# Optimization experiments

Hardware: AMD Instinct MI355X
Metric: run time of the kernel (lower is better)

Reference implementation:

```python
import jax, jax.numpy as jnp
import numpy as np

DIM = 128
N_ITER = 8
L_SIZE = 80000
C_SIZE = 120000
N_EDGES = 480000


def _mlp(x, w1, b1, w2, b2):
    # 2-layer MLP with ReLU (satbench_n_mlp_layers=2, activation='relu')
    return jnp.maximum(x @ w1 + b1, 0.0) @ w2 + b2


def _layer_norm(x, g, b, eps=1e-5):
    mu = jnp.mean(x, axis=-1, keepdims=True)
    var = jnp.var(x, axis=-1, keepdims=True)
    return (x - mu) * jax.lax.rsqrt(var + eps) * g + b


def _ln_lstm_cell(x, h, c, wi, wh, g_ih, b_ih, g_hh, b_hh, g_c, b_c):
    # LayerNormBasicLSTMCell: LN on input/hidden gate pre-activations and on new cell state
    gates = _layer_norm(x @ wi, g_ih, b_ih) + _layer_norm(h @ wh, g_hh, b_hh)
    i, f, g, o = jnp.split(gates, 4, axis=1)
    new_c = jax.nn.sigmoid(f) * c + jax.nn.sigmoid(i) * jnp.tanh(g)
    new_h = jax.nn.sigmoid(o) * jnp.tanh(_layer_norm(new_c, g_c, b_c))
    return new_h, new_c


def setup_inputs() -> dict:
    key = jax.random.key(0)
    ks = jax.random.split(key, 24)
    d = DIM
    s1 = 1.0 / np.sqrt(d)
    s2 = 1.0 / np.sqrt(2 * d)
    inp = {
        'l_size': L_SIZE,
        'c_size': C_SIZE,
        'l_edge_index': jax.random.randint(ks[0], (N_EDGES,), 0, L_SIZE),
        'c_edge_index': jax.random.randint(ks[1], (N_EDGES,), 0, C_SIZE),
        'l_emb': jax.random.normal(ks[2], (L_SIZE, d), jnp.float32),
        'c_emb': jax.random.normal(ks[3], (C_SIZE, d), jnp.float32),
        # l2c message MLP
        'l2c_w1': jax.random.normal(ks[4], (d, d), jnp.float32) * s1,
        'l2c_b1': jnp.zeros((d,), jnp.float32),
        'l2c_w2': jax.random.normal(ks[5], (d, d), jnp.float32) * s1,
        'l2c_b2': jnp.zeros((d,), jnp.float32),
        # c2l message MLP
        'c2l_w1': jax.random.normal(ks[6], (d, d), jnp.float32) * s1,
        'c2l_b1': jnp.zeros((d,), jnp.float32),
        'c2l_w2': jax.random.normal(ks[7], (d, d), jnp.float32) * s1,
        'c2l_b2': jnp.zeros((d,), jnp.float32),
        # clause update LSTM (input=d)
        'cu_wi': jax.random.normal(ks[8], (d, 4 * d), jnp.float32) * s1,
        'cu_wh': jax.random.normal(ks[9], (d, 4 * d), jnp.float32) * s1,
        'cu_g_ih': jnp.ones((4 * d,), jnp.float32),
        'cu_b_ih': jnp.zeros((4 * d,), jnp.float32),
        'cu_g_hh': jnp.ones((4 * d,), jnp.float32),
        'cu_b_hh': jnp.zeros((4 * d,), jnp.float32),
        'cu_g_c': jnp.ones((d,), jnp.float32),
        'cu_b_c': jnp.zeros((d,), jnp.float32),
        # literal update LSTM (input=2*d)
        'lu_wi': jax.random.normal(ks[10], (2 * d, 4 * d), jnp.float32) * s2,
        'lu_wh': jax.random.normal(ks[11], (d, 4 * d), jnp.float32) * s1,
        'lu_g_ih': jnp.ones((4 * d,), jnp.float32),
        'lu_b_ih': jnp.zeros((4 * d,), jnp.float32),
        'lu_g_hh': jnp.ones((4 * d,), jnp.float32),
        'lu_b_hh': jnp.zeros((4 * d,), jnp.float32),
        'lu_g_c': jnp.ones((d,), jnp.float32),
        'lu_b_c': jnp.zeros((d,), jnp.float32),
    }
    return inp


def reference(l_size, c_size, l_edge_index, c_edge_index, l_emb, c_emb,
              l2c_w1, l2c_b1, l2c_w2, l2c_b2,
              c2l_w1, c2l_b1, c2l_w2, c2l_b2,
              cu_wi, cu_wh, cu_g_ih, cu_b_ih, cu_g_hh, cu_b_hh, cu_g_c, cu_b_c,
              lu_wi, lu_wh, lu_g_ih, lu_b_ih, lu_g_hh, lu_b_hh, lu_g_c, lu_b_c):
    d = l_emb.shape[1]
    l_state = jnp.zeros((l_size, d), l_emb.dtype)
    c_state = jnp.zeros((c_size, d), c_emb.dtype)
    l_embs = [l_emb]
    c_embs = [c_emb]
    for _ in range(N_ITER):
        # literal -> clause
        l_msg_feat = _mlp(l_emb, l2c_w1, l2c_b1, l2c_w2, l2c_b2)
        l2c_msg = l_msg_feat[l_edge_index]                             # [E, d] gather
        l2c_aggr = jax.ops.segment_sum(l2c_msg, c_edge_index, num_segments=c_size)
        c_emb, c_state = _ln_lstm_cell(l2c_aggr, c_emb, c_state,
                                       cu_wi, cu_wh, cu_g_ih, cu_b_ih,
                                       cu_g_hh, cu_b_hh, cu_g_c, cu_b_c)
        c_embs.append(c_emb)
        # clause -> literal
        c_msg_feat = _mlp(c_emb, c2l_w1, c2l_b1, c2l_w2, c2l_b2)
        c2l_msg = c_msg_feat[c_edge_index]
        c2l_aggr = jax.ops.segment_sum(c2l_msg, l_edge_index, num_segments=l_size)
        # flip pos/neg literal embeddings (l2l message)
        pl, ul = jnp.split(l_emb.reshape(l_size // 2, 2 * d), 2, axis=1)
        l2l_msg = jnp.concatenate([ul, pl], axis=1).reshape(l_size, d)
        l_emb, l_state = _ln_lstm_cell(jnp.concatenate([c2l_aggr, l2l_msg], axis=1),
                                       l_emb, l_state,
                                       lu_wi, lu_wh, lu_g_ih, lu_b_ih,
                                       lu_g_hh, lu_b_hh, lu_g_c, lu_b_c)
        l_embs.append(l_emb)
    return jnp.stack(l_embs), jnp.stack(c_embs)
```

## Files before the change

### kernel.cpp

```cpp
#include <hip/hip_runtime.h>
#include <hip/hip_bf16.h>

#define L_SIZE 80000
#define C_SIZE 120000
#define N_EDGES 480000
#define DIM 128
#define GDIM 512
#define N_ITER 8
#define MAXDEG 64

typedef __attribute__((ext_vector_type(8))) short short8;
typedef __attribute__((ext_vector_type(4))) float f32x4;

__device__ __forceinline__ ushort f2bf(float f) {
    uint u = __float_as_uint(f);
    u = u + 0x7FFFu + ((u >> 16) & 1u);
    return (ushort)(u >> 16);
}
__device__ __forceinline__ float bf2f(ushort h) {
    return __uint_as_float(((uint)h) << 16);
}
__device__ __forceinline__ void split2(float f, short& hi, short& lo) {
    uint u = __float_as_uint(f);
    hi = (short)(u >> 16);
    float r = f - __uint_as_float(u & 0xFFFF0000u);
    lo = (short)(__float_as_uint(r) >> 16);
}
__device__ __forceinline__ float sigmf(float x) { return 1.f / (1.f + __expf(-x)); }
__device__ __forceinline__ float tanh_f(float x) {
    float e = __expf(2.f * x);
    return 1.f - 2.f / (e + 1.f);
}
__device__ __forceinline__ f32x4 fzero4() {
    f32x4 v; v[0] = v[1] = v[2] = v[3] = 0.f; return v;
}

__global__ __launch_bounds__(256) void fill_ell(
    const int* __restrict__ src, const int* __restrict__ dst,
    int* __restrict__ cnt, int* __restrict__ ell)
{
    int i = blockIdx.x * 256 + threadIdx.x;
    int d = dst[i];
    int pos = atomicAdd(&cnt[d], 1);
    ell[(size_t)d * MAXDEG + pos] = src[i];
}

__global__ __launch_bounds__(256) void pack_w2(const float* __restrict__ W,
                                               ushort* __restrict__ Ph,
                                               ushort* __restrict__ Pl, int K, int N)
{
    int NC = N / 16;
    int total = K * N;
    for (int o = blockIdx.x * 256 + threadIdx.x; o < total; o += gridDim.x * 256) {
        int j = o & 7, hi = (o >> 3) & 3, c = (o >> 5) & 15;
        int rest = o >> 9;
        int cc = rest % NC, ks = rest / NC;
        int row = ks * 32 + hi * 8 + j, col = cc * 16 + c;
        float v = W[(size_t)row * N + col];
        ushort h = f2bf(v);
        Ph[o] = h;
        Pl[o] = f2bf(v - bf2f(h));
    }
}

__device__ __forceinline__ void stageA2(const float* __restrict__ src, int rowBase,
                                        ushort* dst, int tid, int nrows)
{
    const int planeB = nrows * 256;
    for (int idx = tid * 8; idx < nrows * 128; idx += 512 * 8) {
        int r = idx >> 7, k8 = idx & 127;
        const float* p = src + (size_t)(rowBase + r) * DIM + k8;
        float4 v0 = *(const float4*)p;
        float4 v1 = *(const float4*)(p + 4);
        float f[8] = {v0.x, v0.y, v0.z, v0.w, v1.x, v1.y, v1.z, v1.w};
        short8 hi8, lo8;
        #pragma unroll
        for (int j = 0; j < 8; ++j) {
            short h, l;
            split2(f[j], h, l);
            hi8[j] = h;
            lo8[j] = l;
        }
        int boff = r * 256 + ((k8 * 2) ^ ((r & 7) << 4));
        *(short8*)((char*)dst + boff) = hi8;
        *(short8*)((char*)dst + planeB + boff) = lo8;
    }
}

__device__ __forceinline__ short8 readA(const ushort* As, int mi, int k0, int lane)
{
    int r = mi * 16 + (lane & 15);
    int kb = (k0 * 2 + ((lane >> 4) << 4)) ^ ((r & 7) << 4);
    return *(const short8*)((const char*)As + r * 256 + kb);
}

__device__ __forceinline__ short8 readAf(const ushort* As, int mi, int k0, int lane)
{
    int r = (mi * 16 + (lane & 15)) ^ 1;
    int kb = (k0 * 2 + ((lane >> 4) << 4)) ^ ((r & 7) << 4);
    return *(const short8*)((const char*)As + r * 256 + kb);
}

__device__ __forceinline__ short8 readB(const ushort* P, int ks, int NC, int cc,
                                        int laneOff)
{
    return *(const short8*)((const char*)P + (((size_t)(ks * NC + cc)) << 10) + laneOff);
}

#define MFMA3(acc, ah, al, bh, bl)                                              \
    acc = __builtin_amdgcn_mfma_f32_16x16x32_bf16(ah, bh, acc, 0, 0, 0);        \
    acc = __builtin_amdgcn_mfma_f32_16x16x32_bf16(ah, bl, acc, 0, 0, 0);        \
    acc = __builtin_amdgcn_mfma_f32_16x16x32_bf16(al, bh, acc, 0, 0, 0);

__global__ __launch_bounds__(512, 4) void mlp_kernel(
    const float* __restrict__ A,
    const ushort* __restrict__ w1Ph, const ushort* __restrict__ w1Pl,
    const float* __restrict__ b1,
    const ushort* __restrict__ w2Ph, const ushort* __restrict__ w2Pl,
    const float* __restrict__ b2,
    float* __restrict__ msg)
{
    __shared__ __align__(16) ushort AsIn[2 * 64 * 128];
    __shared__ __align__(16) ushort AsHid[2 * 64 * 128];
    const int tid = threadIdx.x;
    const int wv = tid >> 6, lane = tid & 63;
    const int cl = lane & 15, hi = lane >> 4;
    const int rowBase = blockIdx.x * 64;
    const int laneOff = (cl * 4 + hi) * 16;
    const int col = wv * 16 + cl;

    stageA2(A, rowBase, AsIn, tid, 64);
    float b1c = b1[col], b2c = b2[col];
    __syncthreads();

    f32x4 acc[4];
    #pragma unroll
    for (int mi = 0; mi < 4; ++mi) acc[mi] = fzero4();
    #pragma unroll
    for (int ks = 0; ks < 4; ++ks) {
        short8 bh = readB(w1Ph, ks, 8, wv, laneOff);
        short8 bl = readB(w1Pl, ks, 8, wv, laneOff);
        #pragma unroll
        for (int mi = 0; mi < 4; ++mi) {
            short8 ah = readA(AsIn, mi, ks * 32, lane);
            short8 al = readA(AsIn + 64 * 128, mi, ks * 32, lane);
            MFMA3(acc[mi], ah, al, bh, bl);
        }
    }
    #pragma unroll
    for (int mi = 0; mi < 4; ++mi)
        #pragma unroll
        for (int q = 0; q < 4; ++q) {
            int row = mi * 16 + hi * 4 + q;
            float v = fmaxf(acc[mi][q] + b1c, 0.f);
            short h2, l2;
            split2(v, h2, l2);
            int boff = row * 256 + ((2 * col) ^ ((row & 7) << 4));
            *(short*)((char*)AsHid + boff) = h2;
            *(short*)((char*)AsHid + 64 * 256 + boff) = l2;
        }
    __syncthreads();

    f32x4 acc2[4];
    #pragma unroll
    for (int mi = 0; mi < 4; ++mi) acc2[mi] = fzero4();
    #pragma unroll
    for (int ks = 0; ks < 4; ++ks) {
        short8 bh = readB(w2Ph, ks, 8, wv, laneOff);
        short8 bl = readB(w2Pl, ks, 8, wv, laneOff);
        #pragma unroll
        for (int mi = 0; mi < 4; ++mi) {
            short8 ah = readA(AsHid, mi, ks * 32, lane);
            short8 al = readA(AsHid + 64 * 128, mi, ks * 32, lane);
            MFMA3(acc2[mi], ah, al, bh, bl);
        }
    }
    #pragma unroll
    for (int mi = 0; mi < 4; ++mi)
        #pragma unroll
        for (int q = 0; q < 4; ++q) {
            int row = mi * 16 + hi * 4 + q;
            msg[(size_t)(rowBase + row) * DIM + col] = acc2[mi][q] + b2c;
        }
}

template<int KX>
__global__ __launch_bounds__(512, 4) void lstm_kernel(
    const float* __restrict__ msg, const int* __restrict__ cnt,
    const int* __restrict__ ell,
    const float* __restrict__ Hsrc,
    const ushort* __restrict__ wiPh, const ushort* __restrict__ wiPl,
    const ushort* __restrict__ whPh, const ushort* __restrict__ whPl,
    const float* __restrict__ g_ih, const float* __restrict__ b_ih,
    const float* __restrict__ g_hh, const float* __restrict__ b_hh,
    const float* __restrict__ g_c,  const float* __restrict__ b_c,
    float* __restrict__ c_state, float* __restrict__ h_out)
{
    __shared__ __align__(16) ushort AsX0[2 * 32 * 128];
    __shared__ __align__(16) ushort AsH [2 * 32 * 128];
    __shared__ float Cs[32][132];
    __shared__ float red4f[32 * 33];
    __shared__ float lnstf[32 * 4];
    __shared__ float red2f[32 * 17];
    __shared__ float lncf[32 * 2];

    const int tid = threadIdx.x;
    const int wv = tid >> 6, lane = tid & 63;
    const int cl = lane & 15, hi = lane >> 4;
    const int rowBase = blockIdx.x * 32;
    const int laneOff = (cl * 4 + hi) * 16;
    const int d = wv * 16 + cl;

    stageA2(Hsrc, rowBase, AsH, tid, 32);
    {
        #pragma unroll
        for (int idx = tid * 4; idx < 32 * 128; idx += 512 * 4) {
            int r = idx >> 7, c = idx & 127;
            *(float4*)&Cs[r][c] =
                *(const float4*)(c_state + (size_t)(rowBase + r) * DIM + c);
        }
    }

    {
        int r = tid >> 4;
        int d8 = (tid & 15) << 3;
        int row = rowBase + r;
        int deg = cnt[row];
        const int* sl = ell + (size_t)row * MAXDEG;
        float a0=0,a1=0,a2=0,a3=0,a4=0,a5=0,a6=0,a7=0;
        for (int k = 0; k < deg; k += 4) {
            int i0 = sl[k], i1 = sl[k+1], i2 = sl[k+2], i3 = sl[k+3];
            const float* m0 = msg + (size_t)i0 * DIM + d8;
            const float* m1 = msg + (size_t)i1 * DIM + d8;
            const float* m2 = msg + (size_t)i2 * DIM + d8;
            const float* m3 = msg + (size_t)i3 * DIM + d8;
            float4 p00 = *(const float4*)m0,       p01 = *(const float4*)(m0 + 4);
            float4 p10 = *(const float4*)m1,       p11 = *(const float4*)(m1 + 4);
            float4 p20 = *(const float4*)m2,       p21 = *(const float4*)(m2 + 4);
            float4 p30 = *(const float4*)m3,       p31 = *(const float4*)(m3 + 4);
            float w1 = (k + 1 < deg) ? 1.f : 0.f;
            float w2 = (k + 2 < deg) ? 1.f : 0.f;
            float w3 = (k + 3 < deg) ? 1.f : 0.f;
            a0 += p00.x; a1 += p00.y; a2 += p00.z; a3 += p00.w;
            a4 += p01.x; a5 += p01.y; a6 += p01.z; a7 += p01.w;
            a0 += w1 * p10.x; a1 += w1 * p10.y; a2 += w1 * p10.z; a3 += w1 * p10.w;
            a4 += w1 * p11.x; a5 += w1 * p11.y; a6 += w1 * p11.z; a7 += w1 * p11.w;
            a0 += w2 * p20.x; a1 += w2 * p20.y; a2 += w2 * p20.z; a3 += w2 * p20.w;
            a4 += w2 * p21.x; a5 += w2 * p21.y; a6 += w2 * p21.z; a7 += w2 * p21.w;
            a0 += w3 * p30.x; a1 += w3 * p30.y; a2 += w3 * p30.z; a3 += w3 * p30.w;
            a4 += w3 * p31.x; a5 += w3 * p31.y; a6 += w3 * p31.z; a7 += w3 * p31.w;
        }
        float f[8] = {a0,a1,a2,a3,a4,a5,a6,a7};
        short8 hi8, lo8;
        #pragma unroll
        for (int j = 0; j < 8; ++j) {
            short h, l;
            split2(f[j], h, l);
            hi8[j] = h;
            lo8[j] = l;
        }
        int boff = r * 256 + ((d8 * 2) ^ ((r & 7) << 4));
        *(short8*)((char*)AsX0 + boff) = hi8;
        *(short8*)((char*)AsX0 + 32 * 256 + boff) = lo8;
    }

    float gih[4], bih[4], ghh[4], bhh[4];
    #pragma unroll
    for (int jb = 0; jb < 4; ++jb) {
        int col = jb * 128 + d;
        gih[jb] = g_ih[col]; bih[jb] = b_ih[col];
        ghh[jb] = g_hh[col]; bhh[jb] = b_hh[col];
    }
    const float gcv = g_c[d], bcv = b_c[d];
    __syncthreads();

    f32x4 xacc[2][4], hacc[2][4];
    #pragma unroll
    for (int mi = 0; mi < 2; ++mi)
        #pragma unroll
        for (int jb = 0; jb < 4; ++jb) { xacc[mi][jb] = fzero4(); hacc[mi][jb] = fzero4(); }

    #pragma unroll
    for (int ks = 0; ks < KX; ++ks) {
        int k0 = (ks & 3) * 32;
        short8 axh0, axl0, axh1, axl1;
        if (KX == 8 && ks >= 4) {
            axh0 = readAf(AsH, 0, k0, lane);
            axl0 = readAf(AsH + 32 * 128, 0, k0, lane);
            axh1 = readAf(AsH, 1, k0, lane);
            axl1 = readAf(AsH + 32 * 128, 1, k0, lane);
        } else {
            axh0 = readA(AsX0, 0, k0, lane);
            axl0 = readA(AsX0 + 32 * 128, 0, k0, lane);
            axh1 = readA(AsX0, 1, k0, lane);
            axl1 = readA(AsX0 + 32 * 128, 1, k0, lane);
        }
        #pragma unroll
        for (int jb = 0; jb < 4; ++jb) {
            short8 bh = readB(wiPh, ks, 32, jb * 8 + wv, laneOff);
            short8 bl = readB(wiPl, ks, 32, jb * 8 + wv, laneOff);
            MFMA3(xacc[0][jb], axh0, axl0, bh, bl);
            MFMA3(xacc[1][jb], axh1, axl1, bh, bl);
        }
        if (ks < 4) {
            short8 ahh0 = readA(AsH, 0, k0, lane);
            short8 ahl0 = readA(AsH + 32 * 128, 0, k0, lane);
            short8 ahh1 = readA(AsH, 1, k0, lane);
            short8 ahl1 = readA(AsH + 32 * 128, 1, k0, lane);
            #pragma unroll
            for (int jb = 0; jb < 4; ++jb) {
                short8 bh = readB(whPh, ks, 32, jb * 8 + wv, laneOff);
                short8 bl = readB(whPl, ks, 32, jb * 8 + wv, laneOff);
                MFMA3(hacc[0][jb], ahh0, ahl0, bh, bl);
                MFMA3(hacc[1][jb], ahh1, ahl1, bh, bl);
            }
        }
    }

    #pragma unroll
    for (int mi = 0; mi < 2; ++mi)
        #pragma unroll
        for (int q = 0; q < 4; ++q) {
            float px = 0.f, pqx = 0.f, ph = 0.f, pqh = 0.f;
            #pragma unroll
            for (int jb = 0; jb < 4; ++jb) {
                float v = xacc[mi][jb][q]; px += v; pqx += v * v;
                float u = hacc[mi][jb][q]; ph += u; pqh += u * u;
            }
            #pragma unroll
            for (int m = 1; m < 16; m <<= 1) {
                px += __shfl_xor(px, m); pqx += __shfl_xor(pqx, m);
                ph += __shfl_xor(ph, m); pqh += __shfl_xor(pqh, m);
            }
            if (cl == 0) {
                int row = mi * 16 + hi * 4 + q;
                float* rp = red4f + row * 33 + wv * 4;
                rp[0] = px; rp[1] = pqx; rp[2] = ph; rp[3] = pqh;
            }
        }
    __syncthreads();
    if (tid < 32) {
        float sx = 0.f, qx = 0.f, sh = 0.f, qh = 0.f;
        const float* rp = red4f + tid * 33;
        for (int ww = 0; ww < 8; ++ww) {
            sx += rp[ww * 4 + 0]; qx += rp[ww * 4 + 1];
            sh += rp[ww * 4 + 2]; qh += rp[ww * 4 + 3];
        }
        const float inv = 1.f / 512.f;
        float mux = sx * inv, muh = sh * inv;
        lnstf[tid * 4 + 0] = mux;
        lnstf[tid * 4 + 1] = rsqrtf(qx * inv - mux * mux + 1e-5f);
        lnstf[tid * 4 + 2] = muh;
        lnstf[tid * 4 + 3] = rsqrtf(qh * inv - muh * muh + 1e-5f);
    }
    __syncthreads();

    float cn[2][4], og[2][4];
    #pragma unroll
    for (int mi = 0; mi < 2; ++mi)
        #pragma unroll
        for (int q = 0; q < 4; ++q) {
            int row = mi * 16 + hi * 4 + q;
            float mux = lnstf[row * 4 + 0], rx = lnstf[row * 4 + 1];
            float muh = lnstf[row * 4 + 2], rh = lnstf[row * 4 + 3];
            float g4[4];
            #pragma unroll
            for (int jb = 0; jb < 4; ++jb)
                g4[jb] = (xacc[mi][jb][q] - mux) * rx * gih[jb] + bih[jb]
                       + (hacc[mi][jb][q] - muh) * rh * ghh[jb] + bhh[jb];
            float cp = Cs[row][d];
            float cv = sigmf(g4[1]) * cp + sigmf(g4[0]) * tanh_f(g4[2]);
            cn[mi][q] = cv; og[mi][q] = g4[3];
            float sc = cv, qc = cv * cv;
            #pragma unroll
            for (int m = 1; m < 16; m <<= 1) {
                sc += __shfl_xor(sc, m); qc += __shfl_xor(qc, m);
            }
            if (cl == 0) {
                float* rp = red2f + row * 17 + wv * 2;
                rp[0] = sc; rp[1] = qc;
            }
        }
    __syncthreads();
    if (tid < 32) {
        float sc = 0.f, qc = 0.f;
        const float* rp = red2f + tid * 17;
        for (int ww = 0; ww < 8; ++ww) { sc += rp[ww * 2]; qc += rp[ww * 2 + 1]; }
        const float inv = 1.f / 128.f;
        float mu = sc * inv;
        lncf[tid * 2 + 0] = mu;
        lncf[tid * 2 + 1] = rsqrtf(qc * inv - mu * mu + 1e-5f);
    }
    __syncthreads();

    #pragma unroll
    for (int mi = 0; mi < 2; ++mi)
        #pragma unroll
        for (int q = 0; q < 4; ++q) {
            int row = mi * 16 + hi * 4 + q;
            size_t go = (size_t)(rowBase + row) * DIM + d;
            float cv = cn[mi][q];
            float hv = sigmf(og[mi][q]) *
                       tanh_f((cv - lncf[row * 2]) * lncf[row * 2 + 1] * gcv + bcv);
            c_state[go] = cv;
            h_out[go] = hv;
        }
}

extern "C" void kernel_launch(void* const* d_in, const int* in_sizes, int n_in,
                              void* d_out, int out_size, void* d_ws, size_t ws_size,
                              hipStream_t stream)
{
    const int*   l_edge  = (const int*)d_in[2];
    const int*   c_edge  = (const int*)d_in[3];
    const float* l_emb0  = (const float*)d_in[4];
    const float* c_emb0  = (const float*)d_in[5];
    const float* l2c_w1  = (const float*)d_in[6];
    const float* l2c_b1  = (const float*)d_in[7];
    const float* l2c_w2  = (const float*)d_in[8];
    const float* l2c_b2  = (const float*)d_in[9];
    const float* c2l_w1  = (const float*)d_in[10];
    const float* c2l_b1  = (const float*)d_in[11];
    const float* c2l_w2  = (const float*)d_in[12];
    const float* c2l_b2  = (const float*)d_in[13];
    const float* cu_wi   = (const float*)d_in[14];
    const float* cu_wh   = (const float*)d_in[15];
    const float* cu_g_ih = (const float*)d_in[16];
    const float* cu_b_ih = (const float*)d_in[17];
    const float* cu_g_hh = (const float*)d_in[18];
    const float* cu_b_hh = (const float*)d_in[19];
    const float* cu_g_c  = (const float*)d_in[20];
    const float* cu_b_c  = (const float*)d_in[21];
    const float* lu_wi   = (const float*)d_in[22];
    const float* lu_wh   = (const float*)d_in[23];
    const float* lu_g_ih = (const float*)d_in[24];
    const float* lu_b_ih = (const float*)d_in[25];
    const float* lu_g_hh = (const float*)d_in[26];
    const float* lu_b_hh = (const float*)d_in[27];
    const float* lu_g_c  = (const float*)d_in[28];
    const float* lu_b_c  = (const float*)d_in[29];

    float* out = (float*)d_out;
    float* l_slab = out;
    float* c_slab = out + (size_t)9 * L_SIZE * DIM;

    char* wp = (char*)d_ws;
    float*  l_state = (float*)wp;  wp += (size_t)L_SIZE * DIM * 4;
    float*  c_state = (float*)wp;  wp += (size_t)C_SIZE * DIM * 4;
    float*  msg     = (float*)wp;  wp += (size_t)C_SIZE * DIM * 4;
    int* c_cnt = (int*)wp; wp += C_SIZE * 4;
    int* l_cnt = (int*)wp; wp += L_SIZE * 4;
    int* c_ell = (int*)wp; wp += (size_t)C_SIZE * MAXDEG * 4;
    int* l_ell = (int*)wp; wp += (size_t)L_SIZE * MAXDEG * 4;
    ushort* l2c_w1Ph = (ushort*)wp; wp += 128 * 128 * 2;
    ushort* l2c_w1Pl = (ushort*)wp; wp += 128 * 128 * 2;
    ushort* l2c_w2Ph = (ushort*)wp; wp += 128 * 128 * 2;
    ushort* l2c_w2Pl = (ushort*)wp; wp += 128 * 128 * 2;
    ushort* c2l_w1Ph = (ushort*)wp; wp += 128 * 128 * 2;
    ushort* c2l_w1Pl = (ushort*)wp; wp += 128 * 128 * 2;
    ushort* c2l_w2Ph = (ushort*)wp; wp += 128 * 128 * 2;
    ushort* c2l_w2Pl = (ushort*)wp; wp += 128 * 128 * 2;
    ushort* cu_wiPh  = (ushort*)wp; wp += 128 * 512 * 2;
    ushort* cu_wiPl  = (ushort*)wp; wp += 128 * 512 * 2;
    ushort* cu_whPh  = (ushort*)wp; wp += 128 * 512 * 2;
    ushort* cu_whPl  = (ushort*)wp; wp += 128 * 512 * 2;
    ushort* lu_wiPh  = (ushort*)wp; wp += 256 * 512 * 2;
    ushort* lu_wiPl  = (ushort*)wp; wp += 256 * 512 * 2;
    ushort* lu_whPh  = (ushort*)wp; wp += 128 * 512 * 2;
    ushort* lu_whPl  = (ushort*)wp; wp += 128 * 512 * 2;

    const int eb = N_EDGES / 256;

    hipMemsetAsync(c_cnt, 0, C_SIZE * 4, stream);
    hipMemsetAsync(l_cnt, 0, L_SIZE * 4, stream);
    hipMemsetAsync(c_ell, 0, (size_t)C_SIZE * MAXDEG * 4, stream);
    hipMemsetAsync(l_ell, 0, (size_t)L_SIZE * MAXDEG * 4, stream);
    fill_ell<<<eb, 256, 0, stream>>>(l_edge, c_edge, c_cnt, c_ell);
    fill_ell<<<eb, 256, 0, stream>>>(c_edge, l_edge, l_cnt, l_ell);

    pack_w2<<<64, 256, 0, stream>>>(l2c_w1, l2c_w1Ph, l2c_w1Pl, 128, 128);
    pack_w2<<<64, 256, 0, stream>>>(l2c_w2, l2c_w2Ph, l2c_w2Pl, 128, 128);
    pack_w2<<<64, 256, 0, stream>>>(c2l_w1, c2l_w1Ph, c2l_w1Pl, 128, 128);
    pack_w2<<<64, 256, 0, stream>>>(c2l_w2, c2l_w2Ph, c2l_w2Pl, 128, 128);
    pack_w2<<<256, 256, 0, stream>>>(cu_wi, cu_wiPh, cu_wiPl, 128, 512);
    pack_w2<<<256, 256, 0, stream>>>(cu_wh, cu_whPh, cu_whPl, 128, 512);
    pack_w2<<<512, 256, 0, stream>>>(lu_wi, lu_wiPh, lu_wiPl, 256, 512);
    pack_w2<<<256, 256, 0, stream>>>(lu_wh, lu_whPh, lu_whPl, 128, 512);

    hipMemcpyAsync(l_slab, l_emb0, (size_t)L_SIZE * DIM * sizeof(float),
                   hipMemcpyDeviceToDevice, stream);
    hipMemcpyAsync(c_slab, c_emb0, (size_t)C_SIZE * DIM * sizeof(float),
                   hipMemcpyDeviceToDevice, stream);
    hipMemsetAsync(l_state, 0, (size_t)L_SIZE * DIM * sizeof(float), stream);
    hipMemsetAsync(c_state, 0, (size_t)C_SIZE * DIM * sizeof(float), stream);

    for (int t = 0; t < N_ITER; ++t) {
        const float* le = l_slab + (size_t)t * L_SIZE * DIM;
        const float* ce = c_slab + (size_t)t * C_SIZE * DIM;
        float* le1 = l_slab + (size_t)(t + 1) * L_SIZE * DIM;
        float* ce1 = c_slab + (size_t)(t + 1) * C_SIZE * DIM;

        mlp_kernel<<<L_SIZE / 64, 512, 0, stream>>>(le, l2c_w1Ph, l2c_w1Pl, l2c_b1,
                                                    l2c_w2Ph, l2c_w2Pl, l2c_b2, msg);
        lstm_kernel<4><<<C_SIZE / 32, 512, 0, stream>>>(
            msg, c_cnt, c_ell, ce,
            cu_wiPh, cu_wiPl, cu_whPh, cu_whPl,
            cu_g_ih, cu_b_ih, cu_g_hh, cu_b_hh, cu_g_c, cu_b_c,
            c_state, ce1);

        mlp_kernel<<<C_SIZE / 64, 512, 0, stream>>>(ce1, c2l_w1Ph, c2l_w1Pl, c2l_b1,
                                                    c2l_w2Ph, c2l_w2Pl, c2l_b2, msg);
        lstm_kernel<8><<<L_SIZE / 32, 512, 0, stream>>>(
            msg, l_cnt, l_ell, le,
            lu_wiPh, lu_wiPl, lu_whPh, lu_whPl,
            lu_g_ih, lu_b_ih, lu_g_hh, lu_b_hh, lu_g_c, lu_b_c,
            l_state, le1);
    }
}
```

Baseline: 5.372 ms.

## Double LSTM row tile to 64 rows to halve weight reloads per row

```diff
diff --git a/kernel.cpp b/kernel.cpp
--- a/kernel.cpp
+++ b/kernel.cpp
@@ -108,9 +108,11 @@
 }
 
 #define MFMA3(acc, ah, al, bh, bl)                                              \
-    acc = __builtin_amdgcn_mfma_f32_16x16x32_bf16(ah, bh, acc, 0, 0, 0);        \
-    acc = __builtin_amdgcn_mfma_f32_16x16x32_bf16(ah, bl, acc, 0, 0, 0);        \
-    acc = __builtin_amdgcn_mfma_f32_16x16x32_bf16(al, bh, acc, 0, 0, 0);
+    do {                                                                        \
+        acc = __builtin_amdgcn_mfma_f32_16x16x32_bf16(ah, bh, acc, 0, 0, 0);    \
+        acc = __builtin_amdgcn_mfma_f32_16x16x32_bf16(ah, bl, acc, 0, 0, 0);    \
+        acc = __builtin_amdgcn_mfma_f32_16x16x32_bf16(al, bh, acc, 0, 0, 0);    \
+    } while (0)
 
 __global__ __launch_bounds__(512, 4) void mlp_kernel(
     const float* __restrict__ A,
@@ -185,7 +187,7 @@
 }
 
 template<int KX>
-__global__ __launch_bounds__(512, 4) void lstm_kernel(
+__global__ __launch_bounds__(512, 2) void lstm_kernel(
     const float* __restrict__ msg, const int* __restrict__ cnt,
     const int* __restrict__ ell,
     const float* __restrict__ Hsrc,
@@ -196,72 +198,69 @@
     const float* __restrict__ g_c,  const float* __restrict__ b_c,
     float* __restrict__ c_state, float* __restrict__ h_out)
 {
-    __shared__ __align__(16) ushort AsX0[2 * 32 * 128];
-    __shared__ __align__(16) ushort AsH [2 * 32 * 128];
-    __shared__ float Cs[32][132];
-    __shared__ float red4f[32 * 33];
-    __shared__ float lnstf[32 * 4];
-    __shared__ float red2f[32 * 17];
-    __shared__ float lncf[32 * 2];
+    __shared__ __align__(16) ushort AsX0[2 * 64 * 128];
+    __shared__ __align__(16) ushort AsH [2 * 64 * 128];
+    __shared__ float red4f[64 * 33];
+    __shared__ float lnstf[64 * 4];
+    __shared__ float red2f[64 * 17];
+    __shared__ float lncf[64 * 2];
 
     const int tid = threadIdx.x;
     const int wv = tid >> 6, lane = tid & 63;
     const int cl = lane & 15, hi = lane >> 4;
-    const int rowBase = blockIdx.x * 32;
+    const int rowBase = blockIdx.x * 64;
     const int laneOff = (cl * 4 + hi) * 16;
     const int d = wv * 16 + cl;
 
-    stageA2(Hsrc, rowBase, AsH, tid, 32);
+    stageA2(Hsrc, rowBase, AsH, tid, 64);
+
     {
-        #pragma unroll
-        for (int idx = tid * 4; idx < 32 * 128; idx += 512 * 4) {
-            int r = idx >> 7, c = idx & 127;
-            *(float4*)&Cs[r][c] =
-                *(const float4*)(c_state + (size_t)(rowBase + r) * DIM + c);
-        }
-    }
-
-    {
-        int r = tid >> 4;
-        int d8 = (tid & 15) << 3;
+        int r = tid >> 3;
+        int d16 = (tid & 7) << 4;
         int row = rowBase + r;
         int deg = cnt[row];
         const int* sl = ell + (size_t)row * MAXDEG;
-        float a0=0,a1=0,a2=0,a3=0,a4=0,a5=0,a6=0,a7=0;
-        for (int k = 0; k < deg; k += 4) {
-            int i0 = sl[k], i1 = sl[k+1], i2 = sl[k+2], i3 = sl[k+3];
-            const float* m0 = msg + (size_t)i0 * DIM + d8;
-            const float* m1 = msg + (size_t)i1 * DIM + d8;
-            const float* m2 = msg + (size_t)i2 * DIM + d8;
-            const float* m3 = msg + (size_t)i3 * DIM + d8;
-            float4 p00 = *(const float4*)m0,       p01 = *(const float4*)(m0 + 4);
-            float4 p10 = *(const float4*)m1,       p11 = *(const float4*)(m1 + 4);
-            float4 p20 = *(const float4*)m2,       p21 = *(const float4*)(m2 + 4);
-            float4 p30 = *(const float4*)m3,       p31 = *(const float4*)(m3 + 4);
+        float a[16];
+        #pragma unroll
+        for (int j = 0; j < 16; ++j) a[j] = 0.f;
+        for (int k = 0; k < deg; k += 2) {
+            int i0 = sl[k], i1 = sl[k + 1];
+            const float* m0 = msg + (size_t)i0 * DIM + d16;
+            const float* m1 = msg + (size_t)i1 * DIM + d16;
+            float4 p00 = *(const float4*)m0,        p01 = *(const float4*)(m0 + 4);
+            float4 p02 = *(const float4*)(m0 + 8),  p03 = *(const float4*)(m0 + 12);
+            float4 p10 = *(const float4*)m1,        p11 = *(const float4*)(m1 + 4);
+            float4 p12 = *(const float4*)(m1 + 8),  p13 = *(const float4*)(m1 + 12);
             float w1 = (k + 1 < deg) ? 1.f : 0.f;
-            float w2 = (k + 2 < deg) ? 1.f : 0.f;
-            float w3 = (k + 3 < deg) ? 1.f : 0.f;
-            a0 += p00.x; a1 += p00.y; a2 += p00.z; a3 += p00.w;
-            a4 += p01.x; a5 += p01.y; a6 += p01.z; a7 += p01.w;
-            a0 += w1 * p10.x; a1 += w1 * p10.y; a2 += w1 * p10.z; a3 += w1 * p10.w;
-            a4 += w1 * p11.x; a5 += w1 * p11.y; a6 += w1 * p11.z; a7 += w1 * p11.w;
-            a0 += w2 * p20.x; a1 += w2 * p20.y; a2 += w2 * p20.z; a3 += w2 * p20.w;
-            a4 += w2 * p21.x; a5 += w2 * p21.y; a6 += w2 * p21.z; a7 += w2 * p21.w;
-            a0 += w3 * p30.x; a1 += w3 * p30.y; a2 += w3 * p30.z; a3 += w3 * p30.w;
-            a4 += w3 * p31.x; a5 += w3 * p31.y; a6 += w3 * p31.z; a7 += w3 * p31.w;
-        }
-        float f[8] = {a0,a1,a2,a3,a4,a5,a6,a7};
-        short8 hi8, lo8;
+            a[0]  += p00.x; a[1]  += p00.y; a[2]  += p00.z; a[3]  += p00.w;
+            a[4]  += p01.x; a[5]  += p01.y; a[6]  += p01.z; a[7]  += p01.w;
+            a[8]  += p02.x; a[9]  += p02.y; a[10] += p02.z; a[11] += p02.w;
+            a[12] += p03.x; a[13] += p03.y; a[14] += p03.z; a[15] += p03.w;
+            a[0]  += w1 * p10.x; a[1]  += w1 * p10.y; a[2]  += w1 * p10.z; a[3]  += w1 * p10.w;
+            a[4]  += w1 * p11.x; a[5]  += w1 * p11.y; a[6]  += w1 * p11.z; a[7]  += w1 * p11.w;
+            a[8]  += w1 * p12.x; a[9]  += w1 * p12.y; a[10] += w1 * p12.z; a[11] += w1 * p12.w;
+            a[12] += w1 * p13.x; a[13] += w1 * p13.y; a[14] += w1 * p13.z; a[15] += w1 * p13.w;
+        }
+        int sw = (r & 7) << 4;
+        short8 hiA, loA, hiB, loB;
         #pragma unroll
         for (int j = 0; j < 8; ++j) {
             short h, l;
-            split2(f[j], h, l);
-            hi8[j] = h;
-            lo8[j] = l;
-        }
-        int boff = r * 256 + ((d8 * 2) ^ ((r & 7) << 4));
-        *(short8*)((char*)AsX0 + boff) = hi8;
-        *(short8*)((char*)AsX0 + 32 * 256 + boff) = lo8;
+            split2(a[j], h, l);
+            hiA[j] = h; loA[j] = l;
+        }
+        #pragma unroll
+        for (int j = 0; j < 8; ++j) {
+            short h, l;
+            split2(a[8 + j], h, l);
+            hiB[j] = h; loB[j] = l;
+        }
+        int b0 = r * 256 + ((d16 * 2) ^ sw);
+        int b1 = r * 256 + (((d16 + 8) * 2) ^ sw);
+        *(short8*)((char*)AsX0 + b0) = hiA;
+        *(short8*)((char*)AsX0 + b1) = hiB;
+        *(short8*)((char*)AsX0 + 64 * 256 + b0) = loA;
+        *(short8*)((char*)AsX0 + 64 * 256 + b1) = loB;
     }
 
     float gih[4], bih[4], ghh[4], bhh[4];
@@ -274,51 +273,56 @@
     const float gcv = g_c[d], bcv = b_c[d];
     __syncthreads();
 
-    f32x4 xacc[2][4], hacc[2][4];
-    #pragma unroll
-    for (int mi = 0; mi < 2; ++mi)
+    f32x4 xacc[4][4], hacc[4][4];
+    #pragma unroll
+    for (int mi = 0; mi < 4; ++mi)
         #pragma unroll
         for (int jb = 0; jb < 4; ++jb) { xacc[mi][jb] = fzero4(); hacc[mi][jb] = fzero4(); }
 
     #pragma unroll
     for (int ks = 0; ks < KX; ++ks) {
         int k0 = (ks & 3) * 32;
-        short8 axh0, axl0, axh1, axl1;
-        if (KX == 8 && ks >= 4) {
-            axh0 = readAf(AsH, 0, k0, lane);
-            axl0 = readAf(AsH + 32 * 128, 0, k0, lane);
-            axh1 = readAf(AsH, 1, k0, lane);
-            axl1 = readAf(AsH + 32 * 128, 1, k0, lane);
-        } else {
-            axh0 = readA(AsX0, 0, k0, lane);
-            axl0 = readA(AsX0 + 32 * 128, 0, k0, lane);
-            axh1 = readA(AsX0, 1, k0, lane);
-            axl1 = readA(AsX0 + 32 * 128, 1, k0, lane);
+        short8 axh[4], axl[4];
+        #pragma unroll
+        for (int mi = 0; mi < 4; ++mi) {
+            if (KX == 8 && ks >= 4) {
+                axh[mi] = readAf(AsH, mi, k0, lane);
+                axl[mi] = readAf(AsH + 64 * 128, mi, k0, lane);
+            } else {
+                axh[mi] = readA(AsX0, mi, k0, lane);
+                axl[mi] = readA(AsX0 + 64 * 128, mi, k0, lane);
+            }
         }
         #pragma unroll
         for (int jb = 0; jb < 4; ++jb) {
             short8 bh = readB(wiPh, ks, 32, jb * 8 + wv, laneOff);
             short8 bl = readB(wiPl, ks, 32, jb * 8 + wv, laneOff);
-            MFMA3(xacc[0][jb], axh0, axl0, bh, bl);
-            MFMA3(xacc[1][jb], axh1, axl1, bh, bl);
+            #pragma unroll
+            for (int mi = 0; mi < 4; ++mi) {
+                MFMA3(xacc[mi][jb], axh[mi], axl[mi], bh, bl);
+            }
         }
         if (ks < 4) {
-            short8 ahh0 = readA(AsH, 0, k0, lane);
-            short8 ahl0 = readA(AsH + 32 * 128, 0, k0, lane);
-            short8 ahh1 = readA(AsH, 1, k0, lane);
-            short8 ahl1 = readA(AsH + 32 * 128, 1, k0, lane);
+            short8 ahh[4], ahl[4];
+            #pragma unroll
+            for (int mi = 0; mi < 4; ++mi) {
+                ahh[mi] = readA(AsH, mi, k0, lane);
+                ahl[mi] = readA(AsH + 64 * 128, mi, k0, lane);
+            }
             #pragma unroll
             for (int jb = 0; jb < 4; ++jb) {
                 short8 bh = readB(whPh, ks, 32, jb * 8 + wv, laneOff);
                 short8 bl = readB(whPl, ks, 32, jb * 8 + wv, laneOff);
-                MFMA3(hacc[0][jb], ahh0, ahl0, bh, bl);
-                MFMA3(hacc[1][jb], ahh1, ahl1, bh, bl);
-            }
-        }
-    }
-
-    #pragma unroll
-    for (int mi = 0; mi < 2; ++mi)
+                #pragma unroll
+                for (int mi = 0; mi < 4; ++mi) {
+                    MFMA3(hacc[mi][jb], ahh[mi], ahl[mi], bh, bl);
+                }
+            }
+        }
+    }
+
+    #pragma unroll
+    for (int mi = 0; mi < 4; ++mi)
         #pragma unroll
         for (int q = 0; q < 4; ++q) {
             float px = 0.f, pqx = 0.f, ph = 0.f, pqh = 0.f;
@@ -339,7 +343,7 @@
             }
         }
     __syncthreads();
-    if (tid < 32) {
+    if (tid < 64) {
         float sx = 0.f, qx = 0.f, sh = 0.f, qh = 0.f;
         const float* rp = red4f + tid * 33;
         for (int ww = 0; ww < 8; ++ww) {
@@ -355,9 +359,9 @@
     }
     __syncthreads();
 
-    float cn[2][4], og[2][4];
-    #pragma unroll
-    for (int mi = 0; mi < 2; ++mi)
+    float cn[4][4], og[4][4];
+    #pragma unroll
+    for (int mi = 0; mi < 4; ++mi)
         #pragma unroll
         for (int q = 0; q < 4; ++q) {
             int row = mi * 16 + hi * 4 + q;
@@ -368,7 +372,7 @@
             for (int jb = 0; jb < 4; ++jb)
                 g4[jb] = (xacc[mi][jb][q] - mux) * rx * gih[jb] + bih[jb]
                        + (hacc[mi][jb][q] - muh) * rh * ghh[jb] + bhh[jb];
-            float cp = Cs[row][d];
+            float cp = c_state[(size_t)(rowBase + row) * DIM + d];
             float cv = sigmf(g4[1]) * cp + sigmf(g4[0]) * tanh_f(g4[2]);
             cn[mi][q] = cv; og[mi][q] = g4[3];
             float sc = cv, qc = cv * cv;
@@ -382,7 +386,7 @@
             }
         }
     __syncthreads();
-    if (tid < 32) {
+    if (tid < 64) {
         float sc = 0.f, qc = 0.f;
         const float* rp = red2f + tid * 17;
         for (int ww = 0; ww < 8; ++ww) { sc += rp[ww * 2]; qc += rp[ww * 2 + 1]; }
@@ -394,7 +398,7 @@
     __syncthreads();
 
     #pragma unroll
-    for (int mi = 0; mi < 2; ++mi)
+    for (int mi = 0; mi < 4; ++mi)
         #pragma unroll
         for (int q = 0; q < 4; ++q) {
             int row = mi * 16 + hi * 4 + q;
@@ -502,7 +506,7 @@
 
         mlp_kernel<<<L_SIZE / 64, 512, 0, stream>>>(le, l2c_w1Ph, l2c_w1Pl, l2c_b1,
                                                     l2c_w2Ph, l2c_w2Pl, l2c_b2, msg);
-        lstm_kernel<4><<<C_SIZE / 32, 512, 0, stream>>>(
+        lstm_kernel<4><<<C_SIZE / 64, 512, 0, stream>>>(
             msg, c_cnt, c_ell, ce,
             cu_wiPh, cu_wiPl, cu_whPh, cu_whPl,
             cu_g_ih, cu_b_ih, cu_g_hh, cu_b_hh, cu_g_c, cu_b_c,
@@ -510,7 +514,7 @@
 
         mlp_kernel<<<C_SIZE / 64, 512, 0, stream>>>(ce1, c2l_w1Ph, c2l_w1Pl, c2l_b1,
                                                     c2l_w2Ph, c2l_w2Pl, c2l_b2, msg);
-        lstm_kernel<8><<<L_SIZE / 32, 512, 0, stream>>>(
+        lstm_kernel<8><<<L_SIZE / 64, 512, 0, stream>>>(
             msg, l_cnt, l_ell, le,
             lu_wiPh, lu_wiPl, lu_whPh, lu_whPl,
             lu_g_ih, lu_b_ih, lu_g_hh, lu_b_hh, lu_g_c, lu_b_c,
```

Measured after the change: 5.331 ms. No clear change (-0.8%).
